# Kernel optimization log

Hardware: AMD Instinct MI355X
Metric: run time of the kernel (lower is better)

## Reference

```python
import jax, jax.numpy as jnp
import numpy as np

N = 2_000_000
REL_DIM = 14
CAN_DIM = 64
N_TYPES = 4


def setup_inputs() -> dict:
    key = jax.random.key(0)
    ka, kb, kia, kib, kw, kbias = jax.random.split(key, 6)
    return {
        "relation_logits_a": jax.random.normal(ka, (N, REL_DIM), dtype=jnp.float32),
        "relation_logits_b": jax.random.normal(kb, (N, REL_DIM), dtype=jnp.float32),
        "frame_type_ids_a": jax.random.randint(kia, (N,), 0, N_TYPES, dtype=jnp.int32),
        "frame_type_ids_b": jax.random.randint(kib, (N,), 0, N_TYPES, dtype=jnp.int32),
        # stacked expert params: W[e] is (REL_DIM, CAN_DIM), b[e] is (CAN_DIM,)
        "W": jax.random.normal(kw, (N_TYPES, REL_DIM, CAN_DIM), dtype=jnp.float32) * 0.26,
        "b": jax.random.normal(kbias, (N_TYPES, CAN_DIM), dtype=jnp.float32) * 0.26,
    }


def _batch_project(x, ids, W, b):
    # x: (N, REL_DIM), ids: (N,) int in [0, N_TYPES)
    # Masked dispatch to 4 tiny linear experts; peak intermediate is (N, CAN_DIM).
    out = jnp.zeros((x.shape[0], CAN_DIM), dtype=x.dtype)
    for e in range(N_TYPES):
        y = x @ W[e] + b[e]                      # (N, CAN_DIM)
        out = out + jnp.where((ids == e)[:, None], y, jnp.zeros((), x.dtype))
    return out


def reference(relation_logits_a, relation_logits_b, frame_type_ids_a, frame_type_ids_b, W, b):
    proj_a = _batch_project(relation_logits_a, frame_type_ids_a, W, b)
    proj_b = _batch_project(relation_logits_b, frame_type_ids_b, W, b)
    # F.mse_loss default reduction='mean'
    diff = proj_a - proj_b
    return jnp.mean(diff * diff)
```

## Files before the change

### kernel.cpp

```cpp
#include <hip/hip_runtime.h>
#include <hip/hip_fp16.h>


#define N_ROWS   2000000
#define N_CHUNKS (N_ROWS / 64)
#define NBLK     4096
#define LDSW     36

typedef _Float16     h8 __attribute__((ext_vector_type(8)));
typedef float        f4 __attribute__((ext_vector_type(4)));
typedef unsigned int u4 __attribute__((ext_vector_type(4)));

__device__ __forceinline__ unsigned int pkrtz(float a, float b) {
    return __builtin_bit_cast(unsigned int, __builtin_amdgcn_cvt_pkrtz(a, b));
}

struct RowRegs {
    float a[14], b[14];
    int ea, eb;
};

__device__ __forceinline__ RowRegs load_chunk(int c, int lane,
        const float* __restrict__ A, const float* __restrict__ B,
        const int* __restrict__ IDA, const int* __restrict__ IDB) {
    RowRegs r;
    const int row = c * 64 + lane;
    const float* ra = A + (size_t)row * 14;
    const float* rb = B + (size_t)row * 14;
    float4 a0 = *(const float4*)(ra + 0);
    float4 a1 = *(const float4*)(ra + 4);
    float4 a2 = *(const float4*)(ra + 8);
    float2 a3 = *(const float2*)(ra + 12);
    float4 b0 = *(const float4*)(rb + 0);
    float4 b1 = *(const float4*)(rb + 4);
    float4 b2 = *(const float4*)(rb + 8);
    float2 b3 = *(const float2*)(rb + 12);
    r.ea = IDA[row];
    r.eb = IDB[row];
    r.a[0]=a0.x; r.a[1]=a0.y; r.a[2]=a0.z; r.a[3]=a0.w;
    r.a[4]=a1.x; r.a[5]=a1.y; r.a[6]=a1.z; r.a[7]=a1.w;
    r.a[8]=a2.x; r.a[9]=a2.y; r.a[10]=a2.z; r.a[11]=a2.w;
    r.a[12]=a3.x; r.a[13]=a3.y;
    r.b[0]=b0.x; r.b[1]=b0.y; r.b[2]=b0.z; r.b[3]=b0.w;
    r.b[4]=b1.x; r.b[5]=b1.y; r.b[6]=b1.z; r.b[7]=b1.w;
    r.b[8]=b2.x; r.b[9]=b2.y; r.b[10]=b2.z; r.b[11]=b2.w;
    r.b[12]=b3.x; r.b[13]=b3.y;
    return r;
}

__device__ __forceinline__ void scatter_chunk(unsigned int* __restrict__ row32,
                                              const RowRegs& r) {
    const u4 z = {0u, 0u, 0u, 0u};
#pragma unroll
    for (int t = 0; t < 8; ++t) ((u4*)row32)[t] = z;
    if (r.ea == r.eb) {
#pragma unroll
        for (int t = 0; t < 7; ++t)
            row32[7 * r.ea + t] = pkrtz(r.a[2*t] - r.b[2*t], r.a[2*t+1] - r.b[2*t+1]);
    } else {
#pragma unroll
        for (int t = 0; t < 7; ++t)
            row32[7 * r.ea + t] = pkrtz(r.a[2*t], r.a[2*t+1]);
#pragma unroll
        for (int t = 0; t < 7; ++t)
            row32[7 * r.eb + t] = pkrtz(-r.b[2*t], -r.b[2*t+1]);
        const unsigned wa = 0x3C00u << ((r.ea & 1) * 16);
        const unsigned wb = 0xBC00u << ((r.eb & 1) * 16);
        const int ja = 28 + (r.ea >> 1), jb = 28 + (r.eb >> 1);
        if (ja == jb) row32[ja] = wa | wb;
        else { row32[ja] = wa; row32[jb] = wb; }
    }
}

__device__ __forceinline__ void compute_chunk(const unsigned int* __restrict__ sbuf,
                                              int sub, int quad, const h8* wf,
                                              float* ls) {
#pragma unroll
    for (int t = 0; t < 4; ++t) {
        const unsigned int* fr = sbuf + (t * 16 + sub) * LDSW + quad * 4;
        u4 lo = *(const u4*)fr;
        u4 hi = *(const u4*)(fr + 16);
        const h8 e0 = __builtin_bit_cast(h8, lo);
        const h8 e1 = __builtin_bit_cast(h8, hi);
#pragma unroll
        for (int ct = 0; ct < 4; ++ct) {
            const f4 z = {0.0f, 0.0f, 0.0f, 0.0f};
            f4 acc = __builtin_amdgcn_mfma_f32_16x16x32_f16(e0, wf[ct * 2 + 0], z, 0, 0, 0);
            acc     = __builtin_amdgcn_mfma_f32_16x16x32_f16(e1, wf[ct * 2 + 1], acc, 0, 0, 0);
#pragma unroll
            for (int rr = 0; rr < 4; ++rr)
                ls[rr] = fmaf(acc[rr], acc[rr], ls[rr]);
        }
    }
}

__global__ void __launch_bounds__(64, 4)
frame_loss(const float* __restrict__ A, const float* __restrict__ B,
           const int* __restrict__ IDA, const int* __restrict__ IDB,
           const float* __restrict__ W, const float* __restrict__ BIAS,
           float* __restrict__ ws)
{
    __shared__ alignas(16) unsigned int s0[64 * LDSW];

    const int lane = threadIdx.x;
    const int sub  = lane & 15;
    const int quad = lane >> 4;

    h8 wf[8];
#pragma unroll
    for (int ct = 0; ct < 4; ++ct)
#pragma unroll
        for (int s = 0; s < 2; ++s) {
            h8 f;
            const int c = ct * 16 + sub;
#pragma unroll
            for (int j = 0; j < 8; ++j) {
                const int k = s * 32 + quad * 8 + j;
                float v = 0.0f;
                if (k < 56)       v = W[k * 64 + c];
                else if (k < 60)  v = BIAS[(k - 56) * 64 + c];
                f[j] = (_Float16)v;
            }
            wf[ct * 2 + s] = f;
        }

    float ls[4] = {0.0f, 0.0f, 0.0f, 0.0f};
    unsigned int* const myrow = s0 + lane * LDSW;
    const int stride = gridDim.x;

    int c = blockIdx.x;
    RowRegs rr = load_chunk(c, lane, A, B, IDA, IDB);
    scatter_chunk(myrow, rr);

    while (true) {
        int n = c + stride;
        bool more = (n < N_CHUNKS);
        if (more) rr = load_chunk(n, lane, A, B, IDA, IDB);
        compute_chunk(s0, sub, quad, wf, ls);
        if (!more) break;
        scatter_chunk(myrow, rr);
        c = n;
    }

    float lsum = ls[0] + ls[1] + ls[2] + ls[3];
#pragma unroll
    for (int off = 32; off > 0; off >>= 1)
        lsum += __shfl_down(lsum, off, 64);
    if (lane == 0)
        ws[blockIdx.x] = lsum;
}

__global__ void __launch_bounds__(256)
reduce_partials(const float* __restrict__ ws, float* __restrict__ out, int nblk)
{
    const int tid = threadIdx.x;
    float s = 0.0f;
    for (int i = tid; i < nblk; i += 256) s += ws[i];
#pragma unroll
    for (int off = 32; off > 0; off >>= 1)
        s += __shfl_down(s, off, 64);
    __shared__ float tmp[4];
    if ((tid & 63) == 0) tmp[tid >> 6] = s;
    __syncthreads();
    if (tid == 0)
        out[0] = (tmp[0] + tmp[1] + tmp[2] + tmp[3]) * (1.0f / 128000000.0f);
}

extern "C" void kernel_launch(void* const* d_in, const int* in_sizes, int n_in,
                              void* d_out, int out_size, void* d_ws, size_t ws_size,
                              hipStream_t stream) {
    const float* A    = (const float*)d_in[0];
    const float* B    = (const float*)d_in[1];
    const int*   IDA  = (const int*)d_in[2];
    const int*   IDB  = (const int*)d_in[3];
    const float* W    = (const float*)d_in[4];
    const float* BIAS = (const float*)d_in[5];
    float* ws  = (float*)d_ws;
    float* out = (float*)d_out;

    const int nblk = (ws_size >= (size_t)NBLK * sizeof(float)) ? NBLK : 2048;

    frame_loss<<<dim3(nblk), dim3(64), 0, stream>>>(A, B, IDA, IDB, W, BIAS, ws);
    reduce_partials<<<dim3(1), dim3(256), 0, stream>>>(ws, out, nblk);
}
```

Before: 272.9 us.

## Coalesce row loads via LDS staging before packing expert slots

Each wavefront now loads its whole 64-row chunk as contiguous 16-byte and 8-byte per-lane vectors, instead of each lane reading its own 56-byte-strided row. The raw data is written to LDS first. Each lane then reads back its row from LDS and packs it into the fp16 expert-slot layout used by the MFMA stage. This aims to improve global memory coalescing and cut register pressure from holding unpacked floats. The cost is extra LDS traffic, and the scatter overwrites the staging area in place, which relies on wavefront lockstep ordering between lanes.

```diff
diff --git a/kernel.cpp b/kernel.cpp
--- a/kernel.cpp
+++ b/kernel.cpp
@@ -10,63 +10,74 @@
 typedef _Float16     h8 __attribute__((ext_vector_type(8)));
 typedef float        f4 __attribute__((ext_vector_type(4)));
 typedef unsigned int u4 __attribute__((ext_vector_type(4)));
+typedef unsigned int u2 __attribute__((ext_vector_type(2)));
 
 __device__ __forceinline__ unsigned int pkrtz(float a, float b) {
     return __builtin_bit_cast(unsigned int, __builtin_amdgcn_cvt_pkrtz(a, b));
 }
 
-struct RowRegs {
-    float a[14], b[14];
+struct RawRegs {
+    u4 a4[3]; u2 a2;
+    u4 b4[3]; u2 b2;
     int ea, eb;
 };
 
-__device__ __forceinline__ RowRegs load_chunk(int c, int lane,
+__device__ __forceinline__ RawRegs load_chunk(int c, int lane,
         const float* __restrict__ A, const float* __restrict__ B,
         const int* __restrict__ IDA, const int* __restrict__ IDB) {
-    RowRegs r;
-    const int row = c * 64 + lane;
-    const float* ra = A + (size_t)row * 14;
-    const float* rb = B + (size_t)row * 14;
-    float4 a0 = *(const float4*)(ra + 0);
-    float4 a1 = *(const float4*)(ra + 4);
-    float4 a2 = *(const float4*)(ra + 8);
-    float2 a3 = *(const float2*)(ra + 12);
-    float4 b0 = *(const float4*)(rb + 0);
-    float4 b1 = *(const float4*)(rb + 4);
-    float4 b2 = *(const float4*)(rb + 8);
-    float2 b3 = *(const float2*)(rb + 12);
-    r.ea = IDA[row];
-    r.eb = IDB[row];
-    r.a[0]=a0.x; r.a[1]=a0.y; r.a[2]=a0.z; r.a[3]=a0.w;
-    r.a[4]=a1.x; r.a[5]=a1.y; r.a[6]=a1.z; r.a[7]=a1.w;
-    r.a[8]=a2.x; r.a[9]=a2.y; r.a[10]=a2.z; r.a[11]=a2.w;
-    r.a[12]=a3.x; r.a[13]=a3.y;
-    r.b[0]=b0.x; r.b[1]=b0.y; r.b[2]=b0.z; r.b[3]=b0.w;
-    r.b[4]=b1.x; r.b[5]=b1.y; r.b[6]=b1.z; r.b[7]=b1.w;
-    r.b[8]=b2.x; r.b[9]=b2.y; r.b[10]=b2.z; r.b[11]=b2.w;
-    r.b[12]=b3.x; r.b[13]=b3.y;
+    RawRegs r;
+    const char* pa = (const char*)A + (size_t)c * 3584;
+    const char* pb = (const char*)B + (size_t)c * 3584;
+#pragma unroll
+    for (int j = 0; j < 3; ++j) {
+        r.a4[j] = *(const u4*)(pa + j * 1024 + lane * 16);
+        r.b4[j] = *(const u4*)(pb + j * 1024 + lane * 16);
+    }
+    r.a2 = *(const u2*)(pa + 3072 + lane * 8);
+    r.b2 = *(const u2*)(pb + 3072 + lane * 8);
+    r.ea = IDA[c * 64 + lane];
+    r.eb = IDB[c * 64 + lane];
     return r;
 }
 
-__device__ __forceinline__ void scatter_chunk(unsigned int* __restrict__ row32,
-                                              const RowRegs& r) {
+__device__ __forceinline__ void stage_write(unsigned int* __restrict__ s, int lane,
+                                            const RawRegs& r) {
+#pragma unroll
+    for (int j = 0; j < 3; ++j) {
+        *(u4*)(s +       j * 256 + lane * 4) = r.a4[j];
+        *(u4*)(s + 896 + j * 256 + lane * 4) = r.b4[j];
+    }
+    *(u2*)(s +       768 + lane * 2) = r.a2;
+    *(u2*)(s + 896 + 768 + lane * 2) = r.b2;
+}
+
+__device__ __forceinline__ void pack_scatter(unsigned int* __restrict__ s, int lane,
+                                             int ea, int eb) {
+    const float* sa = (const float*)s + 14 * lane;
+    const float* sb = (const float*)s + 896 + 14 * lane;
+    unsigned int pa[7], pb[7];
+    const bool same = (ea == eb);
+#pragma unroll
+    for (int t = 0; t < 7; ++t) {
+        float2 av = *(const float2*)(sa + 2 * t);
+        float2 bv = *(const float2*)(sb + 2 * t);
+        float sx = same ? (av.x - bv.x) : av.x;
+        float sy = same ? (av.y - bv.y) : av.y;
+        pa[t] = pkrtz(sx, sy);
+        pb[t] = pkrtz(-bv.x, -bv.y);
+    }
+    unsigned int* row32 = s + lane * LDSW;
     const u4 z = {0u, 0u, 0u, 0u};
 #pragma unroll
     for (int t = 0; t < 8; ++t) ((u4*)row32)[t] = z;
-    if (r.ea == r.eb) {
 #pragma unroll
-        for (int t = 0; t < 7; ++t)
-            row32[7 * r.ea + t] = pkrtz(r.a[2*t] - r.b[2*t], r.a[2*t+1] - r.b[2*t+1]);
-    } else {
+    for (int t = 0; t < 7; ++t) row32[7 * ea + t] = pa[t];
+    if (!same) {
 #pragma unroll
-        for (int t = 0; t < 7; ++t)
-            row32[7 * r.ea + t] = pkrtz(r.a[2*t], r.a[2*t+1]);
-#pragma unroll
-        for (int t = 0; t < 7; ++t)
-            row32[7 * r.eb + t] = pkrtz(-r.b[2*t], -r.b[2*t+1]);
-        const unsigned wa = 0x3C00u << ((r.ea & 1) * 16);
-        const unsigned wb = 0xBC00u << ((r.eb & 1) * 16);
-        const int ja = 28 + (r.ea >> 1), jb = 28 + (r.eb >> 1);
+        for (int t = 0; t < 7; ++t) row32[7 * eb + t] = pb[t];
+        const unsigned wa = 0x3C00u << ((ea & 1) * 16);
+        const unsigned wb = 0xBC00u << ((eb & 1) * 16);
+        const int ja = 28 + (ea >> 1), jb = 28 + (eb >> 1);
         if (ja == jb) row32[ja] = wa | wb;
         else { row32[ja] = wa; row32[jb] = wb; }
     }
@@ -125,12 +136,12 @@
         }
 
     float ls[4] = {0.0f, 0.0f, 0.0f, 0.0f};
-    unsigned int* const myrow = s0 + lane * LDSW;
     const int stride = gridDim.x;
 
     int c = blockIdx.x;
-    RowRegs rr = load_chunk(c, lane, A, B, IDA, IDB);
-    scatter_chunk(myrow, rr);
+    RawRegs rr = load_chunk(c, lane, A, B, IDA, IDB);
+    stage_write(s0, lane, rr);
+    pack_scatter(s0, lane, rr.ea, rr.eb);
 
     while (true) {
         int n = c + stride;
@@ -138,7 +149,8 @@
         if (more) rr = load_chunk(n, lane, A, B, IDA, IDB);
         compute_chunk(s0, sub, quad, wf, ls);
         if (!more) break;
-        scatter_chunk(myrow, rr);
+        stage_write(s0, lane, rr);
+        pack_scatter(s0, lane, rr.ea, rr.eb);
         c = n;
     }
 
```

After: 282.7 us. 3.6% more time.
